# Optimization experiments

Hardware: AMD Instinct MI355X
Metric: run time of the kernel (lower is better)

The kernel has to match this reference:

```python
import jax, jax.numpy as jnp
import numpy as np
from math import factorial

N_SCALES = 4
N_ORI = 4
NA = 9            # spatial_corr_width
H_IMG = 1024
P_REAL = max(2 * N_ORI, 5)


def _polar_grid(H, W):
    ctr_y = int(np.ceil((H + 0.5) / 2)); ctr_x = int(np.ceil((W + 0.5) / 2))
    y = (np.arange(1, H + 1) - ctr_y) / (H / 2.0)
    x = (np.arange(1, W + 1) - ctr_x) / (W / 2.0)
    xr, yr = np.meshgrid(x, y)
    angle = np.arctan2(yr, xr)
    rad = np.sqrt(xr ** 2 + yr ** 2)
    rad[ctr_y - 1, ctr_x - 1] = rad[ctr_y - 1, ctr_x - 2]  # avoid log2(0)
    return np.log2(rad), angle


def _hi(log_rad, shift):
    # raised-cosine sqrt highpass mask: transition over log_rad in [shift-1, shift]
    return np.cos(np.pi / 2.0 * np.clip(log_rad - shift, -1.0, 0.0))


def _lo(log_rad, shift):
    h = _hi(log_rad, shift)
    return np.sqrt(np.clip(1.0 - h * h, 0.0, 1.0))


def _crop(dims):
    # pyrtools-style frequency-domain downsample-by-2 crop indices
    dims = np.asarray(dims)
    ctr = np.ceil((dims + 0.5) / 2).astype(int)
    lodims = np.ceil((dims - 0.5) / 2).astype(int)
    loctr = np.ceil((lodims + 0.5) / 2).astype(int)
    s = ctr - loctr
    return s[0], s[0] + lodims[0], s[1], s[1] + lodims[1]


def _build_pyramid(im):
    """Complex steerable pyramid (frequency-domain), non tight-frame."""
    order = N_ORI - 1
    const = (2.0 ** (2 * order)) * factorial(order) ** 2 / (N_ORI * factorial(2 * order))
    lr, ang = _polar_grid(*im.shape)
    imdft = jnp.fft.fftshift(jnp.fft.fft2(im))
    hipass = jnp.fft.ifft2(jnp.fft.ifftshift(imdft * jnp.asarray(_hi(lr, 0.0), jnp.float32))).real
    lodft = imdft * jnp.asarray(_lo(lr, 0.0), jnp.float32)
    bands, recon_dfts = [], []
    for s in range(N_SCALES):
        recon_dfts.append(lodft)  # spectrum of scales >= s content (partial recon)
        shift = -(s + 1)
        hm = _hi(lr, shift)
        sb = []
        for b in range(N_ORI):
            a = np.mod(ang - np.pi * b / N_ORI + np.pi, 2 * np.pi) - np.pi
            am = 2.0 * np.sqrt(const) * (np.cos(a) ** order) * (np.abs(a) < np.pi / 2)
            banddft = ((-1j) ** order) * lodft * jnp.asarray(hm * am, jnp.float32)
            sb.append(jnp.fft.ifft2(jnp.fft.ifftshift(banddft)))
        bands.append(sb)
        y0, y1, x0, x1 = _crop(lodft.shape)
        lr, ang = lr[y0:y1, x0:x1], ang[y0:y1, x0:x1]
        lodft = lodft[y0:y1, x0:x1] * jnp.asarray(_lo(lr, shift), jnp.float32)
    lowpass = jnp.fft.ifft2(jnp.fft.ifftshift(lodft)).real
    recons = [jnp.fft.ifft2(jnp.fft.ifftshift(d)).real for d in recon_dfts] + [lowpass]
    return hipass, bands, lowpass, recons


def _autocorr(x):
    # central NA x NA window of the autocorrelation, via FFT
    x = x - x.mean()
    H, W = x.shape
    F = jnp.fft.fft2(x)
    p = F.real ** 2 + F.imag ** 2
    ac = jnp.fft.fftshift(jnp.fft.ifft2(p).real) / (H * W)
    lz = NA // 2
    return jax.lax.dynamic_slice(ac, (H // 2 - lz, W // 2 - lz), (NA, NA))


def _skew_kurt(x):
    mu = x.mean()
    c = x - mu
    v = (c * c).mean()
    return (c ** 3).mean() / v ** 1.5, (c ** 4).mean() / v ** 2, v


def _norm_cc(A, B):
    # true cross-correlation of centered columns
    C = A.T @ B / A.shape[0]
    sa = jnp.sqrt((A * A).mean(0)); sb = jnp.sqrt((B * B).mean(0))
    return C / (sa[:, None] * sb[None, :] + 1e-12)


def _expand2(x):
    H, W = x.shape
    F = jnp.fft.fftshift(jnp.fft.fft2(x))
    pad = jnp.zeros((2 * H, 2 * W), F.dtype).at[H // 2:H // 2 + H, W // 2:W // 2 + W].set(F)
    return jnp.fft.ifft2(jnp.fft.ifftshift(pad)) * 4.0


def _ps_stats(image):
    im = image[0, 0]
    hipass, bands, lowpass, recons = _build_pyramid(im)
    sk, ku, var = _skew_kurt(im)
    pix = jnp.stack([im.mean(), var, sk, ku, im.min(), im.max()])
    mags = [[jnp.abs(bands[s][b]) for b in range(N_ORI)] for s in range(N_SCALES)]
    mag_means = jnp.stack([jnp.abs(hipass).mean()]
                          + [mags[s][b].mean() for s in range(N_SCALES) for b in range(N_ORI)]
                          + [jnp.abs(lowpass).mean()])
    mags = [[m - m.mean() for m in row] for row in mags]
    lz = NA // 2
    acm = jnp.zeros((NA, NA, N_SCALES, N_ORI), jnp.float32)
    for s in range(N_SCALES):
        for b in range(N_ORI):
            ac = _autocorr(mags[s][b])
            acm = acm.at[:, :, s, b].set(ac / (ac[lz, lz] + 1e-12))
    acr = jnp.zeros((NA, NA, N_SCALES + 1), jnp.float32)
    skew_r, kurt_r, std_r = [], [], []
    for s, r in enumerate(recons):
        ac = _autocorr(r)
        acr = acr.at[:, :, s].set(ac / (ac[lz, lz] + 1e-12))
        sk_, ku_, v_ = _skew_kurt(r)
        skew_r.append(sk_); kurt_r.append(ku_); std_r.append(jnp.sqrt(v_))
    com = jnp.zeros((N_ORI, N_ORI, N_SCALES + 1), jnp.float32)
    csm = jnp.zeros((N_ORI, N_ORI, N_SCALES), jnp.float32)
    cor = jnp.zeros((P_REAL, P_REAL, N_SCALES + 1), jnp.float32)
    csr = jnp.zeros((2 * N_ORI, P_REAL, N_SCALES), jnp.float32)
    for s in range(N_SCALES):
        M = jnp.stack([m.ravel() for m in mags[s]], 1)                      # (N, Nor) centered magnitudes
        R = jnp.stack([(bands[s][b].real - bands[s][b].real.mean()).ravel()
                       for b in range(N_ORI)], 1)                            # (N, Nor) real parts
        com = com.at[:, :, s].set(_norm_cc(M, M))
        cor = cor.at[:N_ORI, :N_ORI, s].set(_norm_cc(R, R))
        if s < N_SCALES - 1:
            ups = [_expand2(bands[s + 1][b]) for b in range(N_ORI)]
            dp = [u * u / (jnp.abs(u) + 1e-12) for u in ups]                # phase-doubled parents
            Pm = jnp.stack([(jnp.abs(u) - jnp.abs(u).mean()).ravel() for u in ups], 1)
            csm = csm.at[:, :, s].set(_norm_cc(M, Pm))
            RP = jnp.stack([d.real.ravel() for d in dp] + [d.imag.ravel() for d in dp], 1)
            RP = RP - RP.mean(0)
            csr = csr.at[:N_ORI, :2 * N_ORI, s].set(_norm_cc(R, RP))
        else:
            lp = _expand2(lowpass).real
            lp = lp - lp.mean()
            shifts = [lp, jnp.roll(lp, 2, 1), jnp.roll(lp, -2, 1), jnp.roll(lp, 2, 0), jnp.roll(lp, -2, 0)]
            RP = jnp.stack([t.ravel() for t in shifts], 1)                  # 5 shifted lowpass parents
            csr = csr.at[:N_ORI, :5, s].set(_norm_cc(R, RP))
            cor = cor.at[:5, :5, N_SCALES].set(_norm_cc(RP, RP))
    hc = hipass - hipass.mean()
    var_hp = (hc * hc).mean()
    vec = jnp.concatenate([pix, mag_means, acm.ravel(),
                           jnp.stack(skew_r), jnp.stack(kurt_r), acr.ravel(),
                           jnp.stack(std_r), com.ravel(), csm.ravel(),
                           cor.ravel(), csr.ravel(), var_hp[None]])
    return vec[None, None, :].astype(jnp.float32)  # (B=1, C=1, S=2461)


def setup_inputs():
    key = jax.random.key(0)
    return {"image": jax.random.normal(key, (1, 1, H_IMG, H_IMG), jnp.float32)}


def reference(image):
    return _ps_stats(image)
```

## Files before the change

### kernel.cpp

```cpp
#include <hip/hip_runtime.h>
#include <hip/hip_fp16.h>
#include <math.h>

#define PI_F 3.14159265358979323846f

enum { LOP_NONE=0, LOP_R2C, LOP_PAD };
enum { SOP_REAL=0, SOP_HL };

__host__ __device__ constexpr int P4(int a, int b){ return a*4 - a*(a-1)/2 + (b-a); }
__host__ __device__ constexpr int P5(int a, int b){ return a*5 - a*(a-1)/2 + (b-a); }

__device__ __forceinline__ unsigned encf(float f){
  unsigned u = __float_as_uint(f);
  return (u & 0x80000000u) ? ~u : (u | 0x80000000u);
}
__device__ __forceinline__ float decf(unsigned u){
  unsigned b = (u & 0x80000000u) ? (u ^ 0x80000000u) : ~u;
  return __uint_as_float(b);
}
__device__ __forceinline__ float2 cxmul(float2 a, float c, float s){
  return make_float2(c*a.x - s*a.y, c*a.y + s*a.x);
}
__device__ __forceinline__ float2 f2add(float2 a, float2 b){ return make_float2(a.x+b.x, a.y+b.y); }
__device__ __forceinline__ float2 f2sub(float2 a, float2 b){ return make_float2(a.x-b.x, a.y-b.y); }
__device__ __forceinline__ float2 h2f(__half2 h){ return __half22float2(h); }
__device__ __forceinline__ __half2 f2h(float2 f){ return __float22half2_rn(f); }

template<int CNT, int WAVES>
__device__ __forceinline__ void block_reduce_add(float (&acc)[CNT], double* out){
  __shared__ float red[WAVES*CNT];
  int lane = threadIdx.x & 63;
  int wid  = threadIdx.x >> 6;
  #pragma unroll
  for (int k = 0; k < CNT; k++){
    float v = acc[k];
    #pragma unroll
    for (int o = 32; o > 0; o >>= 1) v += __shfl_down(v, o, 64);
    if (lane == 0) red[wid*CNT + k] = v;
  }
  __syncthreads();
  int t = threadIdx.x;
  if (t < CNT){
    double s = 0.0;
    #pragma unroll
    for (int w = 0; w < WAVES; w++) s += (double)red[w*CNT + t];
    atomicAdd(&out[t], s);
  }
  __syncthreads();
}

template<int CNT, int WAVES>
__device__ __forceinline__ void block_reduce_add_sc(float (&acc)[CNT], double* out, float* red){
  __syncthreads();
  int lane = threadIdx.x & 63;
  int wid  = threadIdx.x >> 6;
  #pragma unroll
  for (int k = 0; k < CNT; k++){
    float v = acc[k];
    #pragma unroll
    for (int o = 32; o > 0; o >>= 1) v += __shfl_down(v, o, 64);
    if (lane == 0) red[wid*CNT + k] = v;
  }
  __syncthreads();
  int t = threadIdx.x;
  if (t < CNT){
    double s = 0.0;
    #pragma unroll
    for (int w = 0; w < WAVES; w++) s += (double)red[w*CNT + t];
    atomicAdd(&out[t], s);
  }
}

__device__ __forceinline__ void polar_f(int iy, int ix, float& lr, float& ang){
  float yn = (float)(iy - 512) * (1.f/512.f);
  float xn = (float)(ix - 512) * (1.f/512.f);
  ang = atan2f(yn, xn);
  float rad = (iy == 512 && ix == 512) ? (1.f/512.f) : sqrtf(xn*xn + yn*yn);
  lr = log2f(rad);
}
__device__ __forceinline__ float f_hi(float lr, float shift){
  float v = fminf(fmaxf(lr - shift, -1.f), 0.f);
  return cosf((PI_F*0.5f) * v);
}
__device__ __forceinline__ float f_lo(float lr, float shift){
  float h = f_hi(lr, shift);
  float q = fminf(fmaxf(1.f - h*h, 0.f), 1.f);
  return sqrtf(q);
}
__device__ __forceinline__ float band_am(float ang, int b){
  float a0 = ang - (PI_F*0.25f)*(float)b + PI_F;
  float a = fmodf(a0, 2.f*PI_F);
  if (a < 0.f) a += 2.f*PI_F;
  a -= PI_F;
  float mk = 0.f;
  if (fabsf(a) < PI_F*0.5f){ float c = cosf(a); mk = 1.78885438199983f*c*c*c; }
  return mk;
}

__device__ __forceinline__ void bfly4(float2* v, bool fwd){
  float2 A = f2add(v[0], v[2]), B = f2sub(v[0], v[2]);
  float2 C = f2add(v[1], v[3]), D = f2sub(v[1], v[3]);
  float2 dj = fwd ? make_float2(D.y, -D.x) : make_float2(-D.y, D.x);
  v[0] = f2add(A, C);
  v[1] = f2add(B, dj);
  v[2] = f2sub(A, C);
  v[3] = f2sub(B, dj);
}

template<int N, int T>
__device__ __forceinline__ void fft_rows_body(float2* sm, int t, float dir){
  const bool fwd = (dir < 0.f);
  int Ns = 1;
  if constexpr ((N & 0xAAAAAAAAu) != 0){
    constexpr int NB2 = N/2;
    constexpr int P2 = (NB2 + T - 1)/T;
    float2 a[P2], b[P2];
    #pragma unroll
    for (int p = 0; p < P2; p++){
      int q = t + p*T;
      if (q < NB2){ a[p] = sm[q]; b[p] = sm[q + N/2]; }
    }
    __syncthreads();
    #pragma unroll
    for (int p = 0; p < P2; p++){
      int q = t + p*T;
      if (q < NB2){
        sm[2*q]   = f2add(a[p], b[p]);
        sm[2*q+1] = f2sub(a[p], b[p]);
      }
    }
    __syncthreads();
    Ns = 2;
  }
  constexpr int NB4 = N/4;
  for (; Ns < N; Ns <<= 2){
    float2 v[4];
    int q = t, k = 0;
    if (q < NB4){
      k = q & (Ns - 1);
      #pragma unroll
      for (int r = 0; r < 4; r++) v[r] = sm[q + r*NB4];
      if (k){
        float ang = dir * (PI_F*0.5f) * (float)k / (float)Ns;
        float s1, c1; __sincosf(ang, &s1, &c1);
        float c2 = c1*c1 - s1*s1, s2 = 2.f*c1*s1;
        float c3 = c1*c2 - s1*s2, s3 = c1*s2 + s1*c2;
        v[1] = cxmul(v[1], c1, s1);
        v[2] = cxmul(v[2], c2, s2);
        v[3] = cxmul(v[3], c3, s3);
      }
      bfly4(v, fwd);
    }
    __syncthreads();
    if (q < NB4){
      int dd = ((q - k) << 2) + k;
      sm[dd]        = v[0];
      sm[dd + Ns]   = v[1];
      sm[dd + 2*Ns] = v[2];
      sm[dd + 3*Ns] = v[3];
    }
    __syncthreads();
  }
}

template<int N, int CB, int T>
__device__ __forceinline__ void fft_cols_body(float2* sm, int t, float dir){
  constexpr int LCB = (CB==2)?1:(CB==4)?2:(CB==8)?3:4;
  const bool fwd = (dir < 0.f);
  int Ns = 1;
  if constexpr ((N & 0xAAAAAAAAu) != 0){
    constexpr int NB2 = (N/2)*CB;
    constexpr int P2 = (NB2 + T - 1)/T;
    float2 a[P2], b[P2];
    #pragma unroll
    for (int p = 0; p < P2; p++){
      int q = t + p*T;
      if (q < NB2){
        int c = q & (CB-1), tt = q >> LCB;
        a[p] = sm[tt*CB + c];
        b[p] = sm[(tt + N/2)*CB + c];
      }
    }
    __syncthreads();
    #pragma unroll
    for (int p = 0; p < P2; p++){
      int q = t + p*T;
      if (q < NB2){
        int c = q & (CB-1), tt = q >> LCB;
        sm[(2*tt)*CB + c]   = f2add(a[p], b[p]);
        sm[(2*tt+1)*CB + c] = f2sub(a[p], b[p]);
      }
    }
    __syncthreads();
    Ns = 2;
  }
  constexpr int NB4 = (N/4)*CB;
  constexpr int PB = (NB4 + T - 1)/T;
  for (; Ns < N; Ns <<= 2){
    float2 v[PB][4];
    int kk[PB];
    #pragma unroll
    for (int p = 0; p < PB; p++){
      int q = t + p*T;
      if (q < NB4){
        int c = q & (CB-1), tt = q >> LCB;
        int k = tt & (Ns - 1);
        kk[p] = k;
        #pragma unroll
        for (int r = 0; r < 4; r++) v[p][r] = sm[(tt + r*(N/4))*CB + c];
        if (k){
          float ang = dir * (PI_F*0.5f) * (float)k / (float)Ns;
          float s1, c1; __sincosf(ang, &s1, &c1);
          float c2 = c1*c1 - s1*s1, s2 = 2.f*c1*s1;
          float c3 = c1*c2 - s1*s2, s3 = c1*s2 + s1*c2;
          v[p][1] = cxmul(v[p][1], c1, s1);
          v[p][2] = cxmul(v[p][2], c2, s2);
          v[p][3] = cxmul(v[p][3], c3, s3);
        }
        bfly4(v[p], fwd);
      }
    }
    __syncthreads();
    #pragma unroll
    for (int p = 0; p < PB; p++){
      int q = t + p*T;
      if (q < NB4){
        int c = q & (CB-1), tt = q >> LCB;
        int k = kk[p];
        int dd = ((tt - k) << 2) + k;
        sm[(dd)*CB + c]        = v[p][0];
        sm[(dd + Ns)*CB + c]   = v[p][1];
        sm[(dd + 2*Ns)*CB + c] = v[p][2];
        sm[(dd + 3*Ns)*CB + c] = v[p][3];
      }
    }
    __syncthreads();
  }
}

template<int N>
__global__ __launch_bounds__((N/4 < 64) ? 64 : N/4)
void ps_fft_rows(float2* __restrict__ dst, const void* __restrict__ vsrc,
                 int srcH1, float dir, int xin, int xout, int lop, int srcHalf)
{
  constexpr int T = (N/4 < 64) ? 64 : N/4;
  __shared__ float2 sm[N];
  const int t = threadIdx.x;
  const int l = blockIdx.x;
  float2* dline = dst + (size_t)l*N;
  if (lop == LOP_PAD){
    const int q = N/4;
    const int sl = l - q;
    if (sl < 0 || sl >= srcH1){
      for (int j = t; j < N; j += T) dline[j] = make_float2(0.f, 0.f);
      return;
    }
    if (srcHalf){
      const __half2* s = (const __half2*)vsrc + (size_t)sl*srcH1;
      for (int j = t; j < N; j += T){
        int p = j ^ xin;
        sm[j] = (p >= q && p < q + srcH1) ? h2f(s[p - q]) : make_float2(0.f, 0.f);
      }
    } else {
      const float2* s = (const float2*)vsrc + (size_t)sl*srcH1;
      for (int j = t; j < N; j += T){
        int p = j ^ xin;
        sm[j] = (p >= q && p < q + srcH1) ? s[p - q] : make_float2(0.f, 0.f);
      }
    }
  } else if (lop == LOP_R2C){
    const float* s = (const float*)vsrc + (size_t)l*N;
    for (int j = t; j < N; j += T) sm[j] = make_float2(s[j ^ xin], 0.f);
  } else {
    if (srcHalf){
      const __half2* s = (const __half2*)vsrc + (size_t)l*N;
      for (int j = t; j < N; j += T) sm[j] = h2f(s[j ^ xin]);
    } else {
      const float2* s = (const float2*)vsrc + (size_t)l*N;
      for (int j = t; j < N; j += T) sm[j] = s[j ^ xin];
    }
  }
  __syncthreads();
  fft_rows_body<N, T>(sm, t, dir);
  for (int j = t; j < N; j += T) dline[j ^ xout] = sm[j];
}

template<int N>
__global__ __launch_bounds__((N/4 < 64) ? 64 : N/4)
void ps_fft_rows_m(__half2* __restrict__ h4, __half2* __restrict__ bandD,
                   __half2* __restrict__ tiledD,
                   const __half2* __restrict__ lodS, const __half2* __restrict__ lodS1,
                   int nA, int h4First, int n, int srcH1,
                   int moffB, float shiftB, int moffC, float shiftC, float scale)
{
  constexpr int T = (N/4 < 64) ? 64 : N/4;
  constexpr int XIN = N/2;
  __shared__ float2 sm[N];
  const int t = threadIdx.x;
  const int l = blockIdx.x & (N-1);
  const int img = blockIdx.x / N;

  if (img < nA){
    if (img == 0 && h4First){
      const __half2* s = h4 + (size_t)l*N;
      for (int j = t; j < N; j += T) sm[j] = h2f(s[j ^ XIN]);
    } else {
      const __half2* s = lodS + (size_t)l*N;
      for (int j = t; j < N; j += T) sm[j] = h2f(s[j ^ XIN]);
    }
  } else if (img < nA + 4){
    const int b = img - nA;
    const __half2* s = lodS + (size_t)l*N;
    for (int j = t; j < N; j += T){
      int x = j ^ XIN;
      float lr, ang; polar_f(moffB + l, moffB + x, lr, ang);
      float mf = f_hi(lr, shiftB) * band_am(ang, b);
      float2 v = h2f(s[x]);
      sm[j] = make_float2(-mf*v.y, mf*v.x);
    }
  } else {
    const int b = img - nA - 4;
    const int q = N/4;
    const int sl = l - q;
    if (sl < 0 || sl >= srcH1){
      __half2 z = f2h(make_float2(0.f, 0.f));
      if (tiledD){
        __half2* dl = tiledD + (size_t)img*n;
        for (int j = t; j < N; j += T)
          dl[(size_t)(j >> 3)*(size_t)(N*8) + ((size_t)l << 3) + (j & 7)] = z;
      } else {
        __half2* dl = h4 + (size_t)(img - 4)*n + (size_t)l*N;
        for (int j = t; j < N; j += T) dl[j] = z;
      }
      return;
    }
    const __half2* s = lodS1 + (size_t)sl*srcH1;
    for (int j = t; j < N; j += T){
      int p = j ^ XIN;
      float2 r = make_float2(0.f, 0.f);
      if (p >= q && p < q + srcH1){
        int x = p - q;
        float lr, ang; polar_f(moffC + sl, moffC + x, lr, ang);
        float mf = f_hi(lr, shiftC) * band_am(ang, b);
        float2 v = h2f(s[x]);
        r = make_float2(-mf*v.y, mf*v.x);
      }
      sm[j] = r;
    }
  }
  __syncthreads();
  fft_rows_body<N, T>(sm, t, +1.f);
  if (tiledD){
    __half2* dl = tiledD + (size_t)img*n;
    for (int j = t; j < N; j += T){
      float2 v = sm[j];
      dl[(size_t)(j >> 3)*(size_t)(N*8) + ((size_t)l << 3) + (j & 7)] =
        f2h(make_float2(v.x*scale, v.y*scale));
    }
  } else {
    __half2* dline;
    if (img < nA)          dline = h4 + (size_t)img*n + (size_t)l*N;
    else if (img < nA + 4) dline = bandD + (size_t)(img - nA)*n + (size_t)l*N;
    else                   dline = h4 + (size_t)(img - 4)*n + (size_t)l*N;
    for (int j = t; j < N; j += T){
      float2 v = sm[j];
      dline[j] = f2h(make_float2(v.x*scale, v.y*scale));
    }
  }
}

template<int N, int CB>
__global__ __launch_bounds__(512)
void ps_fft_cols(const float2* __restrict__ src,
                 __half2* __restrict__ hdst, __half2* __restrict__ lodH,
                 float dir, int xin, int xout, float scale,
                 int sop, float* __restrict__ rdst, double* __restrict__ mout)
{
  constexpr int T = 512;
  constexpr int LCB = (CB==2)?1:(CB==4)?2:(CB==8)?3:4;
  constexpr int NE = N*CB;
  __shared__ float2 sm[NE];
  const int t = threadIdx.x;
  const int c0 = blockIdx.x * CB;
  const float2* sbase = src + c0;

  for (int e = t; e < NE; e += T){
    int j = e >> LCB, c = e & (CB - 1);
    sm[e] = sbase[(size_t)(j ^ xin)*N + c];
  }
  __syncthreads();
  fft_cols_body<N, CB, T>(sm, t, dir);

  if (sop == SOP_HL){
    for (int e = t; e < NE; e += T){
      int j = e >> LCB, c = e & (CB - 1);
      int row = j ^ xout, col = c0 + c;
      float lr, ang; polar_f(row, col, lr, ang);
      float lo = f_lo(lr, 0.f), hi = f_hi(lr, 0.f);
      float2 v = sm[j*CB + c];
      size_t o = (size_t)row*N + col;
      hdst[o] = f2h(make_float2(v.x*hi, v.y*hi));
      lodH[o] = f2h(make_float2(v.x*lo, v.y*lo));
    }
    return;
  }
  for (int e = t; e < NE; e += T){
    int j = e >> LCB, c = e & (CB - 1);
    rdst[(size_t)(j ^ xout)*N + c0 + c] = sm[j*CB + c].x * scale;
  }
  if (mout){
    float acc[5] = {0.f,0.f,0.f,0.f,0.f};
    for (int e = t; e < NE; e += T){
      float r = sm[e].x * scale, r2 = r*r;
      acc[0] += r; acc[1] += r2; acc[2] += r2*r; acc[3] += r2*r2; acc[4] += fabsf(r);
    }
    block_reduce_add_sc<5, 8>(acc, mout, (float*)sm);
  }
}

template<int N, int CB>
__global__ __launch_bounds__(512)
void ps_fft_cols_m(__half2* __restrict__ h4, __half2* __restrict__ bandD,
                   const __half2* __restrict__ srcT,
                   int nA, int n,
                   float* __restrict__ rdst, int rimg, int rmask,
                   double* __restrict__ mout, int mstride)
{
  constexpr int T = 512;
  constexpr int LCB = (CB==2)?1:(CB==4)?2:(CB==8)?3:4;
  constexpr int NBK = N / CB;
  constexpr int NE = N*CB;
  constexpr int XIN = N/2;
  __shared__ float2 sm[NE];
  const int t = threadIdx.x;
  const int img = blockIdx.x / NBK;
  const int cg  = blockIdx.x % NBK;
  const int c0 = cg * CB;
  __half2* hbase;
  if (img < nA)          hbase = h4 + (size_t)img*n + c0;
  else if (img < nA + 4) hbase = bandD + (size_t)(img - nA)*n + c0;
  else                   hbase = h4 + (size_t)(img - 4)*n + c0;

  if (srcT){
    const __half2* sb = srcT + (size_t)img*n + (size_t)cg*(size_t)(CB*N);
    for (int e = t; e < NE; e += T){
      int j = e >> LCB, c = e & (CB - 1);
      sm[e] = h2f(sb[((j ^ XIN) << LCB) + c]);
    }
  } else {
    for (int e = t; e < NE; e += T){
      int j = e >> LCB, c = e & (CB - 1);
      sm[e] = h2f(hbase[(size_t)(j ^ XIN)*N + c]);
    }
  }
  __syncthreads();
  fft_cols_body<N, CB, T>(sm, t, +1.f);

  if (img < nA){
    if ((rmask >> img) & 1){
      for (int e = t; e < NE; e += T){
        int j = e >> LCB, c = e & (CB - 1);
        rdst[(size_t)img*(size_t)rimg + (size_t)j*N + c0 + c] = sm[j*CB + c].x;
      }
    }
    float acc[5] = {0.f,0.f,0.f,0.f,0.f};
    for (int e = t; e < NE; e += T){
      float r = sm[e].x, r2 = r*r;
      acc[0] += r; acc[1] += r2; acc[2] += r2*r; acc[3] += r2*r2; acc[4] += fabsf(r);
    }
    block_reduce_add_sc<5, 8>(acc, mout + (size_t)img*mstride, (float*)sm);
  } else {
    float mul = (img < nA + 4) ? 1.f : 4.f;
    for (int e = t; e < NE; e += T){
      int j = e >> LCB, c = e & (CB - 1);
      float2 v = sm[j*CB + c];
      hbase[(size_t)j*N + c] = f2h(make_float2(v.x*mul, v.y*mul));
    }
  }
}

#define MAX_AC_TASKS 9
struct AcTaskTab {
  const void* src[MAX_AC_TASKS];
  int isMag[MAX_AC_TASKS];
  int H[MAX_AC_TASKS];
  int npi[MAX_AC_TASKS];
  int nb[MAX_AC_TASKS];
  int stOff[MAX_AC_TASKS];
  int stStride[MAX_AC_TASKS];
  int blkStart[MAX_AC_TASKS+1];
  int nTasks;
};

__global__ __launch_bounds__(256, 1)
void ps_spat_ac_multi(AcTaskTab tt, double* __restrict__ ST)
{
  __shared__ float tile[40*40];
  const int gb = blockIdx.x;
  int tk = 0;
  while (tk + 1 < tt.nTasks && gb >= tt.blkStart[tk+1]) tk++;
  const int lb  = gb - tt.blkStart[tk];
  const int nb  = tt.nb[tk];
  const int img = lb / nb;
  const int b0  = lb - img*nb;
  const int H = tt.H[tk];
  const int n_per_img = tt.npi[tk];
  const int isMag = tt.isMag[tk];
  const void* vsrc = tt.src[tk];
  const int t = threadIdx.x;
  const int tilesX = H >> 5;
  const int tiles = tilesX * tilesX;
  float acc[41];
  #pragma unroll
  for (int k = 0; k < 41; k++) acc[k] = 0.f;

  for (int tl = b0; tl < tiles; tl += nb){
    int by = tl / tilesX, bx = tl - by*tilesX;
    int y0 = by << 5, x0 = bx << 5;
    __syncthreads();
    for (int e = t; e < 40*40; e += 256){
      int ly = e / 40, lx = e - ly*40;
      int gy = (y0 + ly - 4) & (H - 1);
      int gx = (x0 + lx - 4) & (H - 1);
      float v;
      if (isMag){
        float2 c = h2f(((const __half2*)vsrc)[(size_t)img*n_per_img + (size_t)gy*H + gx]);
        v = sqrtf(c.x*c.x + c.y*c.y);
      } else {
        v = ((const float*)vsrc)[(size_t)img*n_per_img + (size_t)gy*H + gx];
      }
      tile[e] = v;
    }
    __syncthreads();
    for (int p = t; p < 32*32; p += 256){
      int py = p >> 5, px = p & 31;
      const float* row0 = tile + (py+4)*40 + (px+4);
      float c = row0[0];
      #pragma unroll
      for (int dx = 0; dx <= 4; dx++)
        acc[dx] += c * row0[dx];
      #pragma unroll
      for (int dy = 1; dy <= 4; dy++){
        const float* rw = row0 + dy*40;
        #pragma unroll
        for (int dx = -4; dx <= 4; dx++)
          acc[5 + (dy-1)*9 + (dx+4)] += c * rw[dx];
      }
    }
  }
  block_reduce_add<41, 4>(acc, ST + tt.stOff[tk] + (size_t)img*tt.stStride[tk]);
}

__global__ __launch_bounds__(256)
void ps_crop_lo(__half2* dst, const __half2* src, int Hs, int offNew, float shift){
  int Hd = Hs/2;
  int i = blockIdx.x*blockDim.x + threadIdx.x;
  if (i >= Hd*Hd) return;
  int y = i / Hd, x = i - y*Hd;
  float lr, ang; polar_f(offNew + y, offNew + x, lr, ang);
  float mk = f_lo(lr, shift);
  float2 v = h2f(src[(size_t)(y + Hs/4)*Hs + (x + Hs/4)]);
  dst[i] = f2h(make_float2(v.x*mk, v.y*mk));
}

__global__ void ps_init_mm(unsigned* mm){ mm[0] = 0xFFFFFFFFu; mm[1] = 0u; }

__global__ __launch_bounds__(256, 1)
void ps_im_stats(const float4* __restrict__ x4, int n4, double* out, unsigned* mm){
  float acc[4] = {0.f,0.f,0.f,0.f};
  float mn = INFINITY, mx = -INFINITY;
  for (int i = blockIdx.x*blockDim.x + threadIdx.x; i < n4; i += gridDim.x*blockDim.x){
    float4 v = x4[i];
    float a0 = v.x, a1 = v.y, a2 = v.z, a3 = v.w;
    acc[0] += a0 + a1 + a2 + a3;
    acc[1] += a0*a0 + a1*a1 + a2*a2 + a3*a3;
    acc[2] += a0*a0*a0 + a1*a1*a1 + a2*a2*a2 + a3*a3*a3;
    acc[3] += a0*a0*a0*a0 + a1*a1*a1*a1 + a2*a2*a2*a2 + a3*a3*a3*a3;
    mn = fminf(mn, fminf(fminf(a0,a1), fminf(a2,a3)));
    mx = fmaxf(mx, fmaxf(fmaxf(a0,a1), fmaxf(a2,a3)));
  }
  block_reduce_add<4, 4>(acc, out);
  #pragma unroll
  for (int o = 32; o > 0; o >>= 1){
    mn = fminf(mn, __shfl_down(mn, o, 64));
    mx = fmaxf(mx, __shfl_down(mx, o, 64));
  }
  if ((threadIdx.x & 63) == 0){
    atomicMin(&mm[0], encf(mn));
    atomicMax(&mm[1], encf(mx));
  }
}

struct ScaleATab { const __half2* b[4]; int n[4]; };
__global__ __launch_bounds__(256, 1)
void ps_scaleA_multi(ScaleATab tt, double* __restrict__ ST){
  int s = blockIdx.y;
  int n = tt.n[s];
  if ((size_t)blockIdx.x*blockDim.x >= (size_t)n) return;
  const __half2* bb = tt.b[s];
  double* outp = ST + 64 + s*32;
  float acc[28];
  #pragma unroll
  for (int k = 0; k < 28; k++) acc[k] = 0.f;
  for (int i = blockIdx.x*blockDim.x + threadIdx.x; i < n; i += gridDim.x*blockDim.x){
    float2 v0 = h2f(bb[i]), v1 = h2f(bb[(size_t)n + i]),
           v2 = h2f(bb[2*(size_t)n + i]), v3 = h2f(bb[3*(size_t)n + i]);
    float ab[4] = { sqrtf(v0.x*v0.x+v0.y*v0.y), sqrtf(v1.x*v1.x+v1.y*v1.y),
                    sqrtf(v2.x*v2.x+v2.y*v2.y), sqrtf(v3.x*v3.x+v3.y*v3.y) };
    float re[4] = { v0.x, v1.x, v2.x, v3.x };
    #pragma unroll
    for (int a = 0; a < 4; a++){
      #pragma unroll
      for (int c = a; c < 4; c++){
        acc[P4(a,c)]      += ab[a]*ab[c];
        acc[10 + P4(a,c)] += re[a]*re[c];
      }
      acc[20 + a] += ab[a];
      acc[24 + a] += re[a];
    }
  }
  block_reduce_add<28, 4>(acc, outp);
}
__global__ __launch_bounds__(256, 1)
void ps_scaleB(const __half2* __restrict__ u0, const __half2* __restrict__ u1,
               const __half2* __restrict__ u2, const __half2* __restrict__ u3,
               const __half2* __restrict__ s0, const __half2* __restrict__ s1,
               const __half2* __restrict__ s2, const __half2* __restrict__ s3,
               int n, double* out){
  float acc[72];
  #pragma unroll
  for (int k = 0; k < 72; k++) acc[k] = 0.f;
  for (int i = blockIdx.x*blockDim.x + threadIdx.x; i < n; i += gridDim.x*blockDim.x){
    float2 u[4] = { h2f(u0[i]), h2f(u1[i]), h2f(u2[i]), h2f(u3[i]) };
    float2 bb[4] = { h2f(s0[i]), h2f(s1[i]), h2f(s2[i]), h2f(s3[i]) };
    float au[4], dre[4], dim[4], M[4], R[4];
    #pragma unroll
    for (int c = 0; c < 4; c++){
      float xx = u[c].x, yy = u[c].y;
      float mag = sqrtf(xx*xx + yy*yy);
      float den = mag + 1e-12f;
      au[c] = mag;
      dre[c] = (xx*xx - yy*yy)/den;
      dim[c] = (2.f*xx*yy)/den;
      M[c] = sqrtf(bb[c].x*bb[c].x + bb[c].y*bb[c].y);
      R[c] = bb[c].x;
    }
    #pragma unroll
    for (int c = 0; c < 4; c++){
      acc[c]      += au[c];
      acc[4 + c]  += au[c]*au[c];
      acc[24 + c] += dre[c];
      acc[28 + c] += dim[c];
      acc[32 + c] += dre[c]*dre[c];
      acc[36 + c] += dim[c]*dim[c];
    }
    #pragma unroll
    for (int a = 0; a < 4; a++)
      #pragma unroll
      for (int c = 0; c < 4; c++){
        acc[8 + a*4 + c]  += M[a]*au[c];
        acc[40 + a*4 + c] += R[a]*dre[c];
        acc[56 + a*4 + c] += R[a]*dim[c];
      }
  }
  block_reduce_add<72, 4>(acc, out);
}
__global__ __launch_bounds__(256, 1)
void ps_scaleC(const __half2* __restrict__ s0, const __half2* __restrict__ s1,
               const __half2* __restrict__ s2, const __half2* __restrict__ s3,
               const float* __restrict__ lp, int n, double* out){
  float acc[36];
  #pragma unroll
  for (int k = 0; k < 36; k++) acc[k] = 0.f;
  for (int i = blockIdx.x*blockDim.x + threadIdx.x; i < n; i += gridDim.x*blockDim.x){
    int y = i >> 7, x = i & 127;
    float L[5];
    L[0] = lp[i];
    L[1] = lp[(y << 7) | ((x + 126) & 127)];
    L[2] = lp[(y << 7) | ((x + 2) & 127)];
    L[3] = lp[(((y + 126) & 127) << 7) | x];
    L[4] = lp[(((y + 2) & 127) << 7) | x];
    float R[4] = { h2f(s0[i]).x, h2f(s1[i]).x, h2f(s2[i]).x, h2f(s3[i]).x };
    acc[0] += L[0];
    #pragma unroll
    for (int a = 0; a < 5; a++)
      #pragma unroll
      for (int c = a; c < 5; c++)
        acc[1 + P5(a,c)] += L[a]*L[c];
    #pragma unroll
    for (int a = 0; a < 4; a++)
      #pragma unroll
      for (int j = 0; j < 5; j++)
        acc[16 + a*5 + j] += R[a]*L[j];
  }
  block_reduce_add<36, 4>(acc, out);
}

__device__ __forceinline__ double d_ns(int s){ double h = (double)(1024 >> s); return h*h; }
__device__ __forceinline__ void d_moments(const double* Mo, double n,
                                          double& sk, double& ku, double& var){
  double m = Mo[0]/n, e2 = Mo[1]/n, e3 = Mo[2]/n, e4 = Mo[3]/n;
  var = e2 - m*m;
  double c3 = e3 - 3.0*m*e2 + 2.0*m*m*m;
  double c4 = e4 - 4.0*m*e3 + 6.0*m*m*e2 - 3.0*m*m*m*m;
  sk = c3/pow(var,1.5); ku = c4/(var*var);
}
__device__ __forceinline__ int ac_o(int w){
  int dy = w/9 - 4, dx = w - (w/9)*9 - 4;
  int ady = dy, adx = dx;
  if (dy < 0 || (dy == 0 && dx < 0)){ ady = -dy; adx = -dx; }
  return (ady == 0) ? adx : (5 + (ady-1)*9 + (adx+4));
}

__global__ __launch_bounds__(256)
void ps_finalize(const double* __restrict__ ST, const unsigned* __restrict__ MM,
                 float* __restrict__ out, int out_size){
  int idx = blockIdx.x*blockDim.x + threadIdx.x;
  if (idx >= out_size) return;
  const double n0 = 1048576.0;
  double val = 0.0;

  if (idx <= 5){
    if (idx == 4){ out[4] = decf(MM[0]); return; }
    if (idx == 5){ out[5] = decf(MM[1]); return; }
    double sk, ku, v; d_moments(ST, n0, sk, ku, v);
    val = (idx == 0) ? ST[0]/n0 : (idx == 1) ? v : (idx == 2) ? sk : ku;
  } else if (idx == 6){
    val = ST[8]/n0;
  } else if (idx <= 22){
    int i = idx - 7; int s = i >> 2, b = i & 3;
    val = ST[64 + s*32 + 20 + b] / d_ns(s);
  } else if (idx == 23){
    val = ST[10 + 4*6 + 4] / 4096.0;
  } else if (idx <= 1319){
    int i = idx - 24; int w = i >> 4; int j = i & 15;
    int s = j >> 2, b = j & 3;
    double n = d_ns(s);
    const double* R = ST + 752 + j*48;
    double mu = ST[64 + s*32 + 20 + b]/n, mu2 = mu*mu;
    int o = ac_o(w);
    val = (R[o]/n - mu2) / (R[0]/n - mu2 + 1e-12);
  } else if (idx <= 1329){
    int i = idx - 1320; bool kq = (i >= 5); int r = kq ? i - 5 : i;
    double n = (r == 4) ? 4096.0 : d_ns(r);
    double sk, ku, v; d_moments(ST + 10 + r*6, n, sk, ku, v);
    val = kq ? ku : sk;
  } else if (idx <= 1734){
    int i = idx - 1330; int w = i / 5; int r = i - w*5;
    double n = (r == 4) ? 4096.0 : d_ns(r);
    const double* R = ST + 512 + r*48;
    double mu = ST[10 + r*6]/n, mu2 = mu*mu;
    int o = ac_o(w);
    val = (R[o]/n - mu2) / (R[0]/n - mu2 + 1e-12);
  } else if (idx <= 1739){
    int r = idx - 1735;
    double n = (r == 4) ? 4096.0 : d_ns(r);
    double sk, ku, v; d_moments(ST + 10 + r*6, n, sk, ku, v);
    val = sqrt(v);
  } else if (idx <= 1819){
    int i = idx - 1740; int s = i % 5; int q = i / 5; int a = q >> 2, b = q & 3;
    if (s < 4){
      double n = d_ns(s); const double* A = ST + 64 + s*32;
      double ma = A[20+a]/n, mb = A[20+b]/n;
      double caa = A[P4(a,a)]/n - ma*ma, cbb = A[P4(b,b)]/n - mb*mb;
      int lo = a < b ? a : b, hi = a < b ? b : a;
      double cab = A[P4(lo,hi)]/n - ma*mb;
      val = cab / (sqrt(caa)*sqrt(cbb) + 1e-12);
    }
  } else if (idx <= 1883){
    int i = idx - 1820; int s = i & 3; int q = i >> 2; int a = q >> 2, c = q & 3;
    if (s < 3){
      double n = d_ns(s); const double* A = ST + 64 + s*32; const double* B = ST + 192 + s*80;
      double mM = A[20+a]/n; double sdM = sqrt(A[P4(a,a)]/n - mM*mM);
      double mU = B[c]/n;    double sdU = sqrt(B[4+c]/n - mU*mU);
      val = (B[8 + a*4 + c]/n - mM*mU) / (sdM*sdU + 1e-12);
    }
  } else if (idx <= 2203){
    int i = idx - 1884; int s = i % 5; int q = i / 5; int a = q >> 3, b = q & 7;
    if (s < 4){
      if (a < 4 && b < 4){
        double n = d_ns(s); const double* A = ST + 64 + s*32;
        double ma = A[24+a]/n, mb = A[24+b]/n;
        double caa = A[10+P4(a,a)]/n - ma*ma, cbb = A[10+P4(b,b)]/n - mb*mb;
        int lo = a < b ? a : b, hi = a < b ? b : a;
        double cab = A[10+P4(lo,hi)]/n - ma*mb;
        val = cab / (sqrt(caa)*sqrt(cbb) + 1e-12);
      }
    } else {
      if (a < 5 && b < 5){
        const double* C = ST + 432; const double n3 = 16384.0;
        double lb = C[0]/n3;
        double caa = C[1+P5(a,a)]/n3 - lb*lb, cbb = C[1+P5(b,b)]/n3 - lb*lb;
        int lo = a < b ? a : b, hi = a < b ? b : a;
        double cab = C[1+P5(lo,hi)]/n3 - lb*lb;
        val = cab / (sqrt(caa)*sqrt(cbb) + 1e-12);
      }
    }
  } else if (idx <= 2459){
    int i = idx - 2204; int s = i & 3; int q = i >> 2; int a = q >> 3, c = q & 7;
    if (a < 4){
      double n = d_ns(s); const double* A = ST + 64 + s*32;
      double mR = A[24+a]/n; double sdR = sqrt(A[10+P4(a,a)]/n - mR*mR);
      if (s < 3 && c < 8){
        const double* B = ST + 192 + s*80;
        if (c < 4){
          double md = B[24+c]/n; double sd = sqrt(B[32+c]/n - md*md);
          val = (B[40 + a*4 + c]/n - mR*md) / (sdR*sd + 1e-12);
        } else {
          int cc = c - 4;
          double md = B[28+cc]/n; double sd = sqrt(B[36+cc]/n - md*md);
          val = (B[56 + a*4 + cc]/n - mR*md) / (sdR*sd + 1e-12);
        }
      } else if (s == 3 && c < 5){
        const double* C = ST + 432; const double n3 = 16384.0;
        double lb = C[0]/n3;
        double sdL = sqrt(C[1+P5(c,c)]/n3 - lb*lb);
        val = (C[16 + a*5 + c]/n3 - mR*lb) / (sdR*sdL + 1e-12);
      }
    }
  } else {
    val = ST[5]/n0 - (ST[4]/n0)*(ST[4]/n0);
  }
  out[idx] = (float)val;
}

static void rows_s(int H, float2* dst, const void* src, int srcH1,
                   float dir, int xin, int xout, int lop, int srcHalf, hipStream_t st){
  dim3 g(H);
  switch (H){
    case 64:   ps_fft_rows<64>  <<<g, 64,  0, st>>>(dst, src, srcH1, dir, xin, xout, lop, srcHalf); break;
    case 128:  ps_fft_rows<128> <<<g, 64,  0, st>>>(dst, src, srcH1, dir, xin, xout, lop, srcHalf); break;
    case 256:  ps_fft_rows<256> <<<g, 64,  0, st>>>(dst, src, srcH1, dir, xin, xout, lop, srcHalf); break;
    case 512:  ps_fft_rows<512> <<<g, 128, 0, st>>>(dst, src, srcH1, dir, xin, xout, lop, srcHalf); break;
    case 1024: ps_fft_rows<1024><<<g, 256, 0, st>>>(dst, src, srcH1, dir, xin, xout, lop, srcHalf); break;
    default: break;
  }
}
static void cols_s(int H, const float2* src, __half2* hdst, __half2* lodH,
                   float dir, int xin, int xout, float scale,
                   int sop, float* rdst, double* mout, hipStream_t st){
  switch (H){
    case 64:   ps_fft_cols<64,16>  <<<dim3(64/16),  512, 0, st>>>(src, hdst, lodH, dir, xin, xout, scale, sop, rdst, mout); break;
    case 128:  ps_fft_cols<128,16> <<<dim3(128/16), 512, 0, st>>>(src, hdst, lodH, dir, xin, xout, scale, sop, rdst, mout); break;
    case 256:  ps_fft_cols<256,16> <<<dim3(256/16), 512, 0, st>>>(src, hdst, lodH, dir, xin, xout, scale, sop, rdst, mout); break;
    case 512:  ps_fft_cols<512,16> <<<dim3(512/16), 512, 0, st>>>(src, hdst, lodH, dir, xin, xout, scale, sop, rdst, mout); break;
    case 1024: ps_fft_cols<1024,8> <<<dim3(1024/8), 512, 0, st>>>(src, hdst, lodH, dir, xin, xout, scale, sop, rdst, mout); break;
    default: break;
  }
}
static void rows_m(int H, __half2* h4, __half2* bandD, __half2* tiledD,
                   const __half2* lodS, const __half2* lodS1,
                   int nA, int h4First, int nimg, int n, int srcH1,
                   int moffB, float shiftB, int moffC, float shiftC, float scale, hipStream_t st){
  dim3 g(nimg * H);
  switch (H){
    case 128:  ps_fft_rows_m<128> <<<g, 64,  0, st>>>(h4, bandD, tiledD, lodS, lodS1, nA, h4First, n, srcH1, moffB, shiftB, moffC, shiftC, scale); break;
    case 256:  ps_fft_rows_m<256> <<<g, 64,  0, st>>>(h4, bandD, tiledD, lodS, lodS1, nA, h4First, n, srcH1, moffB, shiftB, moffC, shiftC, scale); break;
    case 512:  ps_fft_rows_m<512> <<<g, 128, 0, st>>>(h4, bandD, tiledD, lodS, lodS1, nA, h4First, n, srcH1, moffB, shiftB, moffC, shiftC, scale); break;
    case 1024: ps_fft_rows_m<1024><<<g, 256, 0, st>>>(h4, bandD, tiledD, lodS, lodS1, nA, h4First, n, srcH1, moffB, shiftB, moffC, shiftC, scale); break;
    default: break;
  }
}
static void cols_m(int H, __half2* h4, __half2* bandD, const __half2* srcT,
                   int nA, int nimg, int n,
                   float* rdst, int rimg, int rmask, double* mout, int mstride, hipStream_t st){
  switch (H){
    case 128:  ps_fft_cols_m<128,16> <<<dim3(nimg*(128/16)), 512, 0, st>>>(h4, bandD, srcT, nA, n, rdst, rimg, rmask, mout, mstride); break;
    case 256:  ps_fft_cols_m<256,16> <<<dim3(nimg*(256/16)), 512, 0, st>>>(h4, bandD, srcT, nA, n, rdst, rimg, rmask, mout, mstride); break;
    case 512:  ps_fft_cols_m<512,16> <<<dim3(nimg*(512/16)), 512, 0, st>>>(h4, bandD, srcT, nA, n, rdst, rimg, rmask, mout, mstride); break;
    case 1024: ps_fft_cols_m<1024,8> <<<dim3(nimg*(1024/8)), 512, 0, st>>>(h4, bandD, srcT, nA, n, rdst, rimg, rmask, mout, mstride); break;
    default: break;
  }
}

static inline dim3 gr(int n){ return dim3((n + 255)/256); }
static inline int  rblocks(int n){ int b = (n + 255)/256; return b > 512 ? 512 : b; }

#define FWD (-1.0f)
#define INV (+1.0f)

extern "C" void kernel_launch(void* const* d_in, const int* in_sizes, int n_in,
                              void* d_out, int out_size, void* d_ws, size_t ws_size,
                              hipStream_t stream){
  (void)in_sizes; (void)n_in;
  const float* im = (const float*)d_in[0];
  float* out = (float*)d_out;

  const int Hs[5]   = {1024, 512, 256, 128, 64};
  const int offs[5] = {0, 256, 384, 448, 480};

  char* base = (char*)d_ws;
  size_t off = 0;
  auto carve = [&](size_t bytes)->void*{
    void* r = base + off;
    off = (off + bytes + 255) & ~(size_t)255;
    return r;
  };
  const int n0 = 1024*1024;
  __half2* lod[5];
  for (int s = 0; s < 5; s++) lod[s] = (__half2*)carve((size_t)Hs[s]*Hs[s]*sizeof(__half2));
  __half2* band[4];
  for (int s = 0; s < 4; s++) band[s] = (__half2*)carve((size_t)4*Hs[s]*Hs[s]*sizeof(__half2));
  float* reals0 = (float*)carve((size_t)2*n0*sizeof(float));
  float* recon[5];
  recon[0] = reals0 + n0;
  for (int s = 1; s < 5; s++) recon[s] = (float*)carve((size_t)Hs[s]*Hs[s]*sizeof(float));
  float* lp = (float*)carve(128*128*sizeof(float));
  float2* scrF = (float2*)carve((size_t)n0*sizeof(float2));
  __half2* h4 = (__half2*)carve((size_t)6*n0*sizeof(__half2));
  __half2* hInt = (__half2*)carve((size_t)10*n0*sizeof(__half2));
  double* ST = (double*)carve(2048*sizeof(double));
  unsigned* MM = (unsigned*)carve(64*sizeof(unsigned));
  if (off > ws_size) return;

  hipMemsetAsync(ST, 0, 2048*sizeof(double), stream);
  ps_init_mm<<<1, 1, 0, stream>>>(MM);
  ps_im_stats<<<256, 256, 0, stream>>>((const float4*)im, n0/4, ST + 0, MM);

  rows_s(1024, scrF, im, 0, FWD, 0, 512, LOP_R2C, 0, stream);
  cols_s(1024, scrF, h4, lod[0], FWD, 0, 512, 1.0f, SOP_HL, nullptr, nullptr, stream);

  for (int s = 0; s < 4; s++){
    int H = Hs[s], n = H*H;
    float invn = 1.0f/((float)H*(float)H);
    ps_crop_lo<<<gr((H/2)*(H/2)), 256, 0, stream>>>(lod[s+1], lod[s], H, offs[s+1], -(float)(s+1));
    int nA = (s == 0) ? 2 : 1;
    int nimg = nA + 4 + ((s < 3) ? 4 : 0);
    __half2* tD = (s == 0) ? hInt : nullptr;
    rows_m(H, h4, band[s], tD, lod[s], lod[s+1], nA, (s == 0) ? 1 : 0, nimg, n, Hs[s+1],
           offs[s], -(float)(s+1), offs[s+1], -(float)(s+2), invn, stream);
    float* rT = (s == 0) ? reals0 : recon[s];
    int rimg = (s == 0) ? n0 : 0;
    int rmask = (s == 0) ? 2 : 1;
    double* mT = (s == 0) ? (ST + 4) : (ST + 10 + s*6);
    int mstr = (s == 0) ? 6 : 0;
    cols_m(H, h4, band[s], tD, nA, nimg, n, rT, rimg, rmask, mT, mstr, stream);
    if (s < 3){
      __half2* u = h4 + (size_t)nA*n;
      ps_scaleB<<<rblocks(n), 256, 0, stream>>>(u, u+n, u+2*(size_t)n, u+3*(size_t)n,
                                                band[s], band[s]+n, band[s]+2*(size_t)n, band[s]+3*(size_t)n,
                                                n, ST + 192 + s*80);
    }
  }
  rows_s(64, scrF, lod[4], 0, INV, 32, 0, LOP_NONE, 1, stream);
  cols_s(64, scrF, nullptr, nullptr, INV, 32, 0, 1.0f/4096.f, SOP_REAL, recon[4], ST + 34, stream);
  rows_s(128, scrF, lod[4], 64, INV, 64, 0, LOP_PAD, 1, stream);
  cols_s(128, scrF, nullptr, nullptr, INV, 64, 0, 1.0f/4096.f, SOP_REAL, lp, nullptr, stream);
  ps_scaleC<<<rblocks(16384), 256, 0, stream>>>(band[3], band[3]+16384, band[3]+2*16384, band[3]+3*16384,
                                                lp, 16384, ST + 432);

  {
    AcTaskTab tt{};
    int nt = 0, blk = 0;
    auto addTask = [&](const void* src, int isMag, int H, int nimgs, int stOff){
      int tiles = (H>>5)*(H>>5);
      int nb = tiles < 128 ? tiles : 128;
      tt.src[nt] = src; tt.isMag[nt] = isMag; tt.H[nt] = H; tt.npi[nt] = H*H;
      tt.nb[nt] = nb; tt.stOff[nt] = stOff; tt.stStride[nt] = 48;
      tt.blkStart[nt] = blk; blk += nb*nimgs; nt++;
    };
    addTask(band[0], 1, 1024, 4, 752 + 0*4*48);
    addTask(recon[0], 0, 1024, 1, 512 + 0*48);
    addTask(band[1], 1, 512, 4, 752 + 1*4*48);
    addTask(recon[1], 0, 512, 1, 512 + 1*48);
    addTask(band[2], 1, 256, 4, 752 + 2*4*48);
    addTask(recon[2], 0, 256, 1, 512 + 2*48);
    addTask(band[3], 1, 128, 4, 752 + 3*4*48);
    addTask(recon[3], 0, 128, 1, 512 + 3*48);
    addTask(recon[4], 0, 64, 1, 512 + 4*48);
    tt.blkStart[nt] = blk; tt.nTasks = nt;
    ps_spat_ac_multi<<<dim3(blk), 256, 0, stream>>>(tt, ST);
  }

  {
    ScaleATab ta{};
    for (int s = 0; s < 4; s++){ ta.b[s] = band[s]; ta.n[s] = Hs[s]*Hs[s]; }
    ps_scaleA_multi<<<dim3(512, 4), 256, 0, stream>>>(ta, ST);
  }

  ps_finalize<<<gr(out_size), 256, 0, stream>>>(ST, MM, out, out_size);
}
```

Baseline: 376.6 us.

## Fuse all lowpass crops into one kernel and fold lowpass upsample into scale-3 FFT

Replaces the four per-scale lowpass crop launches with a single kernel that builds all downsampled lowpass spectra directly from the level-0 spectrum, multiplying the cascaded lowpass masks. The expanded lowpass image at scale 3 is now produced as an extra image in the batched row/column FFT pass, without a mask, instead of by a separate 128-point rows/cols FFT pair. This removes several small kernel launches and intermediate round-trips. In exchange, the crop kernel recomputes polar coordinates and up to four masks per pixel, and the half-precision intermediate is skipped, which changes rounding slightly.

```diff
diff --git a/kernel.cpp b/kernel.cpp
--- a/kernel.cpp
+++ b/kernel.cpp
@@ -290,7 +290,7 @@
 void ps_fft_rows_m(__half2* __restrict__ h4, __half2* __restrict__ bandD,
                    __half2* __restrict__ tiledD,
                    const __half2* __restrict__ lodS, const __half2* __restrict__ lodS1,
-                   int nA, int h4First, int n, int srcH1,
+                   int nA, int h4First, int n, int srcH1, int upMask,
                    int moffB, float shiftB, int moffC, float shiftC, float scale)
 {
   constexpr int T = (N/4 < 64) ? 64 : N/4;
@@ -340,10 +340,14 @@
       float2 r = make_float2(0.f, 0.f);
       if (p >= q && p < q + srcH1){
         int x = p - q;
-        float lr, ang; polar_f(moffC + sl, moffC + x, lr, ang);
-        float mf = f_hi(lr, shiftC) * band_am(ang, b);
         float2 v = h2f(s[x]);
-        r = make_float2(-mf*v.y, mf*v.x);
+        if (upMask){
+          float lr, ang; polar_f(moffC + sl, moffC + x, lr, ang);
+          float mf = f_hi(lr, shiftC) * band_am(ang, b);
+          r = make_float2(-mf*v.y, mf*v.x);
+        } else {
+          r = v;
+        }
       }
       sm[j] = r;
     }
@@ -424,7 +428,8 @@
                    const __half2* __restrict__ srcT,
                    int nA, int n,
                    float* __restrict__ rdst, int rimg, int rmask,
-                   double* __restrict__ mout, int mstride)
+                   double* __restrict__ mout, int mstride,
+                   float* __restrict__ lpDst)
 {
   constexpr int T = 512;
   constexpr int LCB = (CB==2)?1:(CB==4)?2:(CB==8)?3:4;
@@ -469,12 +474,24 @@
       acc[0] += r; acc[1] += r2; acc[2] += r2*r; acc[3] += r2*r2; acc[4] += fabsf(r);
     }
     block_reduce_add_sc<5, 8>(acc, mout + (size_t)img*mstride, (float*)sm);
-  } else {
-    float mul = (img < nA + 4) ? 1.f : 4.f;
+  } else if (img < nA + 4){
     for (int e = t; e < NE; e += T){
       int j = e >> LCB, c = e & (CB - 1);
       float2 v = sm[j*CB + c];
-      hbase[(size_t)j*N + c] = f2h(make_float2(v.x*mul, v.y*mul));
+      hbase[(size_t)j*N + c] = f2h(v);
+    }
+  } else {
+    if (lpDst){
+      for (int e = t; e < NE; e += T){
+        int j = e >> LCB, c = e & (CB - 1);
+        lpDst[(size_t)j*N + c0 + c] = sm[j*CB + c].x * 4.f;
+      }
+    } else {
+      for (int e = t; e < NE; e += T){
+        int j = e >> LCB, c = e & (CB - 1);
+        float2 v = sm[j*CB + c];
+        hbase[(size_t)j*N + c] = f2h(make_float2(v.x*4.f, v.y*4.f));
+      }
     }
   }
 }
@@ -552,15 +569,31 @@
 }
 
 __global__ __launch_bounds__(256)
-void ps_crop_lo(__half2* dst, const __half2* src, int Hs, int offNew, float shift){
-  int Hd = Hs/2;
+void ps_crop_all(__half2* __restrict__ l1, __half2* __restrict__ l2,
+                 __half2* __restrict__ l3, __half2* __restrict__ l4,
+                 const __half2* __restrict__ l0)
+{
   int i = blockIdx.x*blockDim.x + threadIdx.x;
-  if (i >= Hd*Hd) return;
-  int y = i / Hd, x = i - y*Hd;
-  float lr, ang; polar_f(offNew + y, offNew + x, lr, ang);
-  float mk = f_lo(lr, shift);
-  float2 v = h2f(src[(size_t)(y + Hs/4)*Hs + (x + Hs/4)]);
-  dst[i] = f2h(make_float2(v.x*mk, v.y*mk));
+  int k, H;
+  if (i < 262144){ k = 1; H = 512; }
+  else if (i < 262144 + 65536){ k = 2; H = 256; i -= 262144; }
+  else if (i < 262144 + 65536 + 16384){ k = 3; H = 128; i -= 262144 + 65536; }
+  else if (i < 262144 + 65536 + 16384 + 4096){ k = 4; H = 64; i -= 262144 + 65536 + 16384; }
+  else return;
+  int y = i / H, x = i - y*H;
+  const int offk = (k==1) ? 256 : (k==2) ? 384 : (k==3) ? 448 : 480;
+  int oy = offk + y, ox = offk + x;
+  float lr, ang; polar_f(oy, ox, lr, ang);
+  float mk = f_lo(lr, -1.f);
+  if (k >= 2) mk *= f_lo(lr, -2.f);
+  if (k >= 3) mk *= f_lo(lr, -3.f);
+  if (k >= 4) mk *= f_lo(lr, -4.f);
+  float2 v = h2f(l0[(size_t)oy*1024 + ox]);
+  __half2 r = f2h(make_float2(v.x*mk, v.y*mk));
+  if (k == 1)      l1[(size_t)y*512 + x] = r;
+  else if (k == 2) l2[(size_t)y*256 + x] = r;
+  else if (k == 3) l3[(size_t)y*128 + x] = r;
+  else             l4[(size_t)y*64  + x] = r;
 }
 
 __global__ void ps_init_mm(unsigned* mm){ mm[0] = 0xFFFFFFFFu; mm[1] = 0u; }
@@ -850,25 +883,26 @@
 }
 static void rows_m(int H, __half2* h4, __half2* bandD, __half2* tiledD,
                    const __half2* lodS, const __half2* lodS1,
-                   int nA, int h4First, int nimg, int n, int srcH1,
+                   int nA, int h4First, int nimg, int n, int srcH1, int upMask,
                    int moffB, float shiftB, int moffC, float shiftC, float scale, hipStream_t st){
   dim3 g(nimg * H);
   switch (H){
-    case 128:  ps_fft_rows_m<128> <<<g, 64,  0, st>>>(h4, bandD, tiledD, lodS, lodS1, nA, h4First, n, srcH1, moffB, shiftB, moffC, shiftC, scale); break;
-    case 256:  ps_fft_rows_m<256> <<<g, 64,  0, st>>>(h4, bandD, tiledD, lodS, lodS1, nA, h4First, n, srcH1, moffB, shiftB, moffC, shiftC, scale); break;
-    case 512:  ps_fft_rows_m<512> <<<g, 128, 0, st>>>(h4, bandD, tiledD, lodS, lodS1, nA, h4First, n, srcH1, moffB, shiftB, moffC, shiftC, scale); break;
-    case 1024: ps_fft_rows_m<1024><<<g, 256, 0, st>>>(h4, bandD, tiledD, lodS, lodS1, nA, h4First, n, srcH1, moffB, shiftB, moffC, shiftC, scale); break;
+    case 128:  ps_fft_rows_m<128> <<<g, 64,  0, st>>>(h4, bandD, tiledD, lodS, lodS1, nA, h4First, n, srcH1, upMask, moffB, shiftB, moffC, shiftC, scale); break;
+    case 256:  ps_fft_rows_m<256> <<<g, 64,  0, st>>>(h4, bandD, tiledD, lodS, lodS1, nA, h4First, n, srcH1, upMask, moffB, shiftB, moffC, shiftC, scale); break;
+    case 512:  ps_fft_rows_m<512> <<<g, 128, 0, st>>>(h4, bandD, tiledD, lodS, lodS1, nA, h4First, n, srcH1, upMask, moffB, shiftB, moffC, shiftC, scale); break;
+    case 1024: ps_fft_rows_m<1024><<<g, 256, 0, st>>>(h4, bandD, tiledD, lodS, lodS1, nA, h4First, n, srcH1, upMask, moffB, shiftB, moffC, shiftC, scale); break;
     default: break;
   }
 }
 static void cols_m(int H, __half2* h4, __half2* bandD, const __half2* srcT,
                    int nA, int nimg, int n,
-                   float* rdst, int rimg, int rmask, double* mout, int mstride, hipStream_t st){
+                   float* rdst, int rimg, int rmask, double* mout, int mstride,
+                   float* lpDst, hipStream_t st){
   switch (H){
-    case 128:  ps_fft_cols_m<128,16> <<<dim3(nimg*(128/16)), 512, 0, st>>>(h4, bandD, srcT, nA, n, rdst, rimg, rmask, mout, mstride); break;
-    case 256:  ps_fft_cols_m<256,16> <<<dim3(nimg*(256/16)), 512, 0, st>>>(h4, bandD, srcT, nA, n, rdst, rimg, rmask, mout, mstride); break;
-    case 512:  ps_fft_cols_m<512,16> <<<dim3(nimg*(512/16)), 512, 0, st>>>(h4, bandD, srcT, nA, n, rdst, rimg, rmask, mout, mstride); break;
-    case 1024: ps_fft_cols_m<1024,8> <<<dim3(nimg*(1024/8)), 512, 0, st>>>(h4, bandD, srcT, nA, n, rdst, rimg, rmask, mout, mstride); break;
+    case 128:  ps_fft_cols_m<128,16> <<<dim3(nimg*(128/16)), 512, 0, st>>>(h4, bandD, srcT, nA, n, rdst, rimg, rmask, mout, mstride, lpDst); break;
+    case 256:  ps_fft_cols_m<256,16> <<<dim3(nimg*(256/16)), 512, 0, st>>>(h4, bandD, srcT, nA, n, rdst, rimg, rmask, mout, mstride, lpDst); break;
+    case 512:  ps_fft_cols_m<512,16> <<<dim3(nimg*(512/16)), 512, 0, st>>>(h4, bandD, srcT, nA, n, rdst, rimg, rmask, mout, mstride, lpDst); break;
+    case 1024: ps_fft_cols_m<1024,8> <<<dim3(nimg*(1024/8)), 512, 0, st>>>(h4, bandD, srcT, nA, n, rdst, rimg, rmask, mout, mstride, lpDst); break;
     default: break;
   }
 }
@@ -920,21 +954,26 @@
   rows_s(1024, scrF, im, 0, FWD, 0, 512, LOP_R2C, 0, stream);
   cols_s(1024, scrF, h4, lod[0], FWD, 0, 512, 1.0f, SOP_HL, nullptr, nullptr, stream);
 
+  ps_crop_all<<<gr(262144 + 65536 + 16384 + 4096), 256, 0, stream>>>(
+      lod[1], lod[2], lod[3], lod[4], lod[0]);
+
   for (int s = 0; s < 4; s++){
     int H = Hs[s], n = H*H;
     float invn = 1.0f/((float)H*(float)H);
-    ps_crop_lo<<<gr((H/2)*(H/2)), 256, 0, stream>>>(lod[s+1], lod[s], H, offs[s+1], -(float)(s+1));
     int nA = (s == 0) ? 2 : 1;
-    int nimg = nA + 4 + ((s < 3) ? 4 : 0);
+    int nups = (s < 3) ? 4 : 1;
+    int nimg = nA + 4 + nups;
+    int upMask = (s < 3) ? 1 : 0;
     __half2* tD = (s == 0) ? hInt : nullptr;
     rows_m(H, h4, band[s], tD, lod[s], lod[s+1], nA, (s == 0) ? 1 : 0, nimg, n, Hs[s+1],
-           offs[s], -(float)(s+1), offs[s+1], -(float)(s+2), invn, stream);
+           upMask, offs[s], -(float)(s+1), offs[s+1], -(float)(s+2), invn, stream);
     float* rT = (s == 0) ? reals0 : recon[s];
     int rimg = (s == 0) ? n0 : 0;
     int rmask = (s == 0) ? 2 : 1;
     double* mT = (s == 0) ? (ST + 4) : (ST + 10 + s*6);
     int mstr = (s == 0) ? 6 : 0;
-    cols_m(H, h4, band[s], tD, nA, nimg, n, rT, rimg, rmask, mT, mstr, stream);
+    float* lpD = (s == 3) ? lp : nullptr;
+    cols_m(H, h4, band[s], tD, nA, nimg, n, rT, rimg, rmask, mT, mstr, lpD, stream);
     if (s < 3){
       __half2* u = h4 + (size_t)nA*n;
       ps_scaleB<<<rblocks(n), 256, 0, stream>>>(u, u+n, u+2*(size_t)n, u+3*(size_t)n,
@@ -944,8 +983,6 @@
   }
   rows_s(64, scrF, lod[4], 0, INV, 32, 0, LOP_NONE, 1, stream);
   cols_s(64, scrF, nullptr, nullptr, INV, 32, 0, 1.0f/4096.f, SOP_REAL, recon[4], ST + 34, stream);
-  rows_s(128, scrF, lod[4], 64, INV, 64, 0, LOP_PAD, 1, stream);
-  cols_s(128, scrF, nullptr, nullptr, INV, 64, 0, 1.0f/4096.f, SOP_REAL, lp, nullptr, stream);
   ps_scaleC<<<rblocks(16384), 256, 0, stream>>>(band[3], band[3]+16384, band[3]+2*16384, band[3]+3*16384,
                                                 lp, 16384, ST + 432);
 
```

After: 364.2 us, median of 2. 1.03x faster.
